# Performance work log

Hardware: AMD Instinct MI355X
Metric: run time of the kernel (lower is better)

The kernel has to match this reference:

```python
import jax, jax.numpy as jnp
import numpy as np

B, L, N, C, H = 32, 11, 577, 768, 12
HD = C // H  # head dim 64
THRESH = 0.5
NEG = -1e9


def layer_norm(x, g, b, eps=1e-6):
    m = jnp.mean(x, axis=-1, keepdims=True)
    v = jnp.var(x, axis=-1, keepdims=True)
    return (x - m) * jax.lax.rsqrt(v + eps) * g + b


def setup_inputs() -> dict:
    key = jax.random.key(0)
    ks = jax.random.split(key, 8)
    s = 0.02
    return {
        "last_x": jax.random.normal(ks[0], (B, N, C), jnp.float32),
        "attn_scores": jax.random.normal(ks[1], (B, L, N), jnp.float32),
        "norm1_g": jnp.ones((C,), jnp.float32),
        "norm1_b": jnp.zeros((C,), jnp.float32),
        "qkv_w": jax.random.normal(ks[2], (3 * C, C), jnp.float32) * s,
        "qkv_b": jnp.zeros((3 * C,), jnp.float32),
        "proj_w": jax.random.normal(ks[3], (C, C), jnp.float32) * s,
        "proj_b": jnp.zeros((C,), jnp.float32),
        "norm2_g": jnp.ones((C,), jnp.float32),
        "norm2_b": jnp.zeros((C,), jnp.float32),
        "fc1_w": jax.random.normal(ks[4], (4 * C, C), jnp.float32) * s,
        "fc1_b": jnp.zeros((4 * C,), jnp.float32),
        "fc2_w": jax.random.normal(ks[5], (C, 4 * C), jnp.float32) * s,
        "fc2_b": jnp.zeros((C,), jnp.float32),
        "bbn_g": jnp.ones((C,), jnp.float32),
        "bbn_b": jnp.zeros((C,), jnp.float32),
        "out_g": jnp.ones((C,), jnp.float32),
        "out_b": jnp.zeros((C,), jnp.float32),
    }


def prune(attn_scores):
    # scores per block, drop CLS column, softmax over patches, mean over blocks
    ps = jax.nn.softmax(attn_scores[:, :, 1:], axis=-1).mean(axis=1)  # [B, P]
    order = jnp.argsort(ps, axis=1)  # ascending
    sorted_s = jnp.take_along_axis(ps, order, axis=1)
    keep_sorted = jnp.cumsum(sorted_s, axis=1) > THRESH  # drop low-mass prefix
    # scatter back to original patch positions
    pm = jnp.zeros_like(keep_sorted)
    pm = pm.at[jnp.arange(ps.shape[0])[:, None], order].set(keep_sorted)
    # CLS token always kept
    return jnp.concatenate([jnp.ones((ps.shape[0], 1), bool), pm], axis=1)  # [B, N]


def masked_block(x, token_masks, norm1_g, norm1_b, qkv_w, qkv_b, proj_w, proj_b,
                 norm2_g, norm2_b, fc1_w, fc1_b, fc2_w, fc2_b):
    b, n, c = x.shape
    h = layer_norm(x, norm1_g, norm1_b)
    qkv = (h @ qkv_w.T + qkv_b).reshape(b, n, 3, H, HD).transpose(2, 0, 3, 1, 4)
    q, k, v = qkv[0], qkv[1], qkv[2]  # [B, H, N, HD]
    att = jnp.einsum("bhqd,bhkd->bhqk", q, k) * (HD ** -0.5)
    mf = token_masks.astype(x.dtype)
    pair = (mf[:, None, :, None] * mf[:, None, None, :]) > 0  # [B,1,N,N]
    att = jnp.where(pair, att, NEG)
    p = jax.nn.softmax(att, axis=-1)
    p = jnp.where(pair, p, 0.0)  # zero fully-masked rows
    y = jnp.einsum("bhqk,bhkd->bhqd", p, v).transpose(0, 2, 1, 3).reshape(b, n, c)
    y = y @ proj_w.T + proj_b
    x = x + y
    m = layer_norm(x, norm2_g, norm2_b)
    m = jax.nn.gelu(m @ fc1_w.T + fc1_b, approximate=False) @ fc2_w.T + fc2_b
    return x + m


def reference(last_x, attn_scores, norm1_g, norm1_b, qkv_w, qkv_b, proj_w, proj_b,
              norm2_g, norm2_b, fc1_w, fc1_b, fc2_w, fc2_b, bbn_g, bbn_b, out_g, out_b):
    token_masks = prune(attn_scores)  # [B, N] bool
    x = masked_block(last_x, token_masks, norm1_g, norm1_b, qkv_w, qkv_b,
                     proj_w, proj_b, norm2_g, norm2_b, fc1_w, fc1_b, fc2_w, fc2_b)
    x = layer_norm(x, bbn_g, bbn_b)  # backbone final norm
    mf = token_masks.astype(x.dtype)
    pooled = (x * mf[:, :, None]).sum(axis=1) / mf.sum(axis=1, keepdims=True)
    return layer_norm(pooled, out_g, out_b)  # [B, C]
```

## Files before the change

### kernel.cpp

```cpp
#include <hip/hip_runtime.h>

#define B_   32
#define L_   11
#define N_   577
#define C_   768
#define H_   12
#define HD_  64
#define M_   (B_ * N_)
#define NP_  608
#define QT_  16
#define NQT_ 37
#define MCH_ 4616

typedef unsigned int uint32;

typedef short bf16x8 __attribute__((ext_vector_type(8)));
typedef float f32x4  __attribute__((ext_vector_type(4)));

__device__ __forceinline__ unsigned short f2bf(float f) {
    union { float f; uint32 u; } c; c.f = f;
    uint32 u = c.u;
    uint32 r = (u + 0x7FFFu + ((u >> 16) & 1u)) >> 16;
    return (unsigned short)r;
}
__device__ __forceinline__ float bf2f(unsigned short u) {
    union { uint32 u; float f; } c; c.u = ((uint32)u) << 16;
    return c.f;
}
__device__ __forceinline__ float ldval(const float* p, size_t i) { return p[i]; }
__device__ __forceinline__ float ldval(const unsigned short* p, size_t i) { return bf2f(p[i]); }

__device__ __forceinline__ bf16x8 ld_frag(const unsigned short* p) {
    union { uint4 u; bf16x8 v; } c;
    c.u = *reinterpret_cast<const uint4*>(p);
    return c.v;
}

__device__ __forceinline__ void gload_lds16(const unsigned short* g, unsigned short* l) {
    __builtin_amdgcn_global_load_lds(
        (const __attribute__((address_space(1))) unsigned int*)g,
        (__attribute__((address_space(3))) unsigned int*)l, 16, 0, 0);
}

__global__ __launch_bounds__(256) void cast4_kernel(const float* __restrict__ qkvw,
                                                    const float* __restrict__ projw,
                                                    const float* __restrict__ fc1w,
                                                    const float* __restrict__ fc2w,
                                                    unsigned short* __restrict__ dq,
                                                    unsigned short* __restrict__ dp,
                                                    unsigned short* __restrict__ d1,
                                                    unsigned short* __restrict__ d2) {
    int i = blockIdx.x * 256 + threadIdx.x;
    const int N0 = 442368, N1 = 147456, N2 = 589824;
    const float* s; unsigned short* d; int j;
    if (i < N0)                { s = qkvw; d = dq; j = i; }
    else if (i < N0 + N1)      { s = projw; d = dp; j = i - N0; }
    else if (i < N0 + N1 + N2) { s = fc1w;  d = d1; j = i - N0 - N1; }
    else                       { s = fc2w;  d = d2; j = i - N0 - N1 - N2; }
    float4 v = reinterpret_cast<const float4*>(s)[j];
    union { unsigned short us[4]; uint2 u; } o;
    o.us[0] = f2bf(v.x); o.us[1] = f2bf(v.y); o.us[2] = f2bf(v.z); o.us[3] = f2bf(v.w);
    reinterpret_cast<uint2*>(d)[j] = o.u;
}

__global__ __launch_bounds__(256) void prune_kernel(const float* __restrict__ scores,
                                                    float* __restrict__ maskf,
                                                    float* __restrict__ cnt) {
    int b = blockIdx.x, tid = threadIdx.x;
    int lane = tid & 63, wave = tid >> 6;
    __shared__ float ps[576];
    __shared__ float red[4];
    for (int j = tid; j < 576; j += 256) ps[j] = 0.f;
    __syncthreads();
    for (int l = 0; l < L_; ++l) {
        const float* row = scores + ((size_t)b * L_ + l) * N_ + 1;
        float mx = -3.4e38f;
        for (int j = tid; j < 576; j += 256) mx = fmaxf(mx, row[j]);
        for (int off = 32; off; off >>= 1) mx = fmaxf(mx, __shfl_xor(mx, off));
        if (lane == 0) red[wave] = mx;
        __syncthreads();
        mx = fmaxf(fmaxf(red[0], red[1]), fmaxf(red[2], red[3]));
        __syncthreads();
        float s = 0.f;
        for (int j = tid; j < 576; j += 256) s += expf(row[j] - mx);
        for (int off = 32; off; off >>= 1) s += __shfl_xor(s, off);
        if (lane == 0) red[wave] = s;
        __syncthreads();
        s = red[0] + red[1] + red[2] + red[3];
        float inv = 1.f / s;
        for (int j = tid; j < 576; j += 256) ps[j] += expf(row[j] - mx) * inv;
        __syncthreads();
    }
    for (int j = tid; j < 576; j += 256) ps[j] = ps[j] / 11.0f;
    __syncthreads();
    int kept = 0;
    for (int i = tid; i < 576; i += 256) {
        float vi = ps[i];
        float s = 0.f;
        for (int j = 0; j < 576; ++j) {
            float vj = ps[j];
            if (vj < vi || (vj == vi && j <= i)) s += vj;
        }
        int k = (s > 0.5f) ? 1 : 0;
        maskf[b * N_ + 1 + i] = (float)k;
        kept += k;
    }
    __syncthreads();
    for (int off = 32; off; off >>= 1) kept += __shfl_xor(kept, off);
    if (lane == 0) red[wave] = (float)kept;
    __syncthreads();
    if (tid == 0) {
        cnt[b] = red[0] + red[1] + red[2] + red[3] + 1.f;
        maskf[b * N_] = 1.f;
    }
}

template<typename T>
__global__ __launch_bounds__(256) void ln_kernel(const T* __restrict__ x,
                                                 const float* __restrict__ g,
                                                 const float* __restrict__ bta,
                                                 unsigned short* __restrict__ dst_bf,
                                                 float* __restrict__ mu_out,
                                                 float* __restrict__ rs_out) {
    int row = blockIdx.x, tid = threadIdx.x;
    int lane = tid & 63, wave = tid >> 6;
    const T* xr = x + (size_t)row * C_;
    __shared__ float s1[4], s2[4];
    float s = 0.f, sq = 0.f;
    for (int c = tid; c < C_; c += 256) { float v = ldval(xr, c); s += v; sq += v * v; }
    for (int off = 32; off; off >>= 1) { s += __shfl_xor(s, off); sq += __shfl_xor(sq, off); }
    if (lane == 0) { s1[wave] = s; s2[wave] = sq; }
    __syncthreads();
    float ts = s1[0] + s1[1] + s1[2] + s1[3];
    float tq = s2[0] + s2[1] + s2[2] + s2[3];
    float mean = ts / (float)C_;
    float var = tq / (float)C_ - mean * mean;
    float rs = rsqrtf(var + 1e-6f);
    if (mu_out && tid == 0) { mu_out[row] = mean; rs_out[row] = rs; }
    if (dst_bf) {
        for (int c = tid; c < C_; c += 256) {
            float v = (ldval(xr, c) - mean) * rs * g[c] + bta[c];
            dst_bf[(size_t)row * C_ + c] = f2bf(v);
        }
    }
}

template<int MODE, int MI>
__global__ __launch_bounds__(256) void gemm_kernel(const unsigned short* __restrict__ A,
                                                   const unsigned short* __restrict__ Bm,
                                                   const float* __restrict__ bias,
                                                   const float* __restrict__ residf,
                                                   const unsigned short* __restrict__ residb,
                                                   unsigned short* __restrict__ outb,
                                                   unsigned short* __restrict__ qd,
                                                   unsigned short* __restrict__ kd,
                                                   unsigned short* __restrict__ vd,
                                                   int M, int N, int K) {
    constexpr int TILE = MI * 32;
    __shared__ unsigned short As[TILE * 32];
    __shared__ unsigned short Bs[TILE * 32];
    int bid = blockIdx.x;
    int NT = N / TILE;
    int mt = bid / NT, nt = bid % NT;
    int m0 = mt * TILE, n0 = nt * TILE;
    int tid = threadIdx.x, lane = tid & 63, wave = tid >> 6;
    int ml = lane & 15, quad = lane >> 4;
    int srow = wave * 16 + (lane >> 2);
    int skc = (lane & 3) * 8;
    const unsigned short* ag[MI / 2 == 0 ? 1 : MI / 2];
    const unsigned short* bg[MI / 2 == 0 ? 1 : MI / 2];
#pragma unroll
    for (int jj = 0; jj < MI / 2; ++jj) {
        ag[jj] = A + (size_t)min(m0 + jj * 64 + srow, M - 1) * K + skc;
        bg[jj] = Bm + (size_t)(n0 + jj * 64 + srow) * K + skc;
    }
    int msub = (wave & 1) * (MI * 16), nsub = (wave >> 1) * (MI * 16);
    f32x4 acc[MI][MI] = {};
    for (int k0 = 0; k0 < K; k0 += 32) {
        __syncthreads();
#pragma unroll
        for (int jj = 0; jj < MI / 2; ++jj) {
            gload_lds16(ag[jj] + k0, As + jj * 2048 + wave * 512);
            gload_lds16(bg[jj] + k0, Bs + jj * 2048 + wave * 512);
        }
        asm volatile("s_waitcnt vmcnt(0)" ::: "memory");
        __syncthreads();
        bf16x8 af[MI], bfm[MI];
#pragma unroll
        for (int i = 0; i < MI; ++i) af[i] = ld_frag(As + (msub + 16 * i + ml) * 32 + quad * 8);
#pragma unroll
        for (int j = 0; j < MI; ++j) bfm[j] = ld_frag(Bs + (nsub + 16 * j + ml) * 32 + quad * 8);
#pragma unroll
        for (int i = 0; i < MI; ++i)
#pragma unroll
            for (int j = 0; j < MI; ++j)
                acc[i][j] = __builtin_amdgcn_mfma_f32_16x16x32_bf16(af[i], bfm[j], acc[i][j], 0, 0, 0);
    }
#pragma unroll
    for (int i = 0; i < MI; ++i)
#pragma unroll
    for (int j = 0; j < MI; ++j)
#pragma unroll
    for (int r = 0; r < 4; ++r) {
        int row = m0 + msub + 16 * i + quad * 4 + r;
        if (row >= M) continue;
        int col = n0 + nsub + 16 * j + ml;
        float v = acc[i][j][r] + bias[col];
        if (MODE == 0) {
            int b = row / N_, t = row - b * N_;
            int f = col;
            if (f < 768) {
                qd[((size_t)(b * H_ + (f >> 6)) * N_ + t) * HD_ + (f & 63)] = f2bf(v * 0.125f);
            } else if (f < 1536) {
                f -= 768;
                kd[((size_t)(b * H_ + (f >> 6)) * N_ + t) * HD_ + (f & 63)] = f2bf(v);
            } else {
                f -= 1536;
                vd[((size_t)(b * H_ + (f >> 6)) * HD_ + (f & 63)) * NP_ + t] = f2bf(v);
            }
        } else if (MODE == 1) {
            outb[(size_t)row * N + col] = f2bf(v + residf[(size_t)row * N + col]);
        } else if (MODE == 2) {
            float gl = 0.5f * v * (1.f + erff(v * 0.70710678118654752f));
            outb[(size_t)row * N + col] = f2bf(gl);
        } else {
            outb[(size_t)row * N + col] = f2bf(v + bf2f(residb[(size_t)row * N + col]));
        }
    }
}

__global__ __launch_bounds__(256, 4) void attn_kernel(const unsigned short* __restrict__ qb,
                                                      const unsigned short* __restrict__ kb,
                                                      const unsigned short* __restrict__ vt,
                                                      const float* __restrict__ maskf,
                                                      unsigned short* __restrict__ ybf) {
    int bid = blockIdx.x;
    int xcd = bid & 7, g = bid >> 3;
    int bh = (g / NQT_) * 8 + xcd;
    int qt = g % NQT_;
    int h = bh % H_, b = bh / H_;
    int q0 = qt * QT_;
    int tid = threadIdx.x, lane = tid & 63, wave = tid >> 6;
    int ml = lane & 15, quad = lane >> 4, kq = quad * 8;
    __shared__ __align__(16) unsigned short P[QT_][616];
    __shared__ float wred[4][QT_];

    const float* bmask = maskf + (size_t)b * N_;
    float mrowv[4];
#pragma unroll
    for (int r = 0; r < 4; ++r) {
        int t = q0 + quad * 4 + r;
        mrowv[r] = (t < N_) ? bmask[t] : 0.f;
    }
    const unsigned short* qbase = qb + (size_t)(b * H_ + h) * N_ * HD_;
    const unsigned short* kbase = kb + (size_t)(b * H_ + h) * N_ * HD_;
    int qrow = min(q0 + ml, N_ - 1);
    bf16x8 aq0 = ld_frag(qbase + (size_t)qrow * HD_ + kq);
    bf16x8 aq1 = ld_frag(qbase + (size_t)qrow * HD_ + kq + 32);
    float sreg[10][4];
    float ls[4] = {0.f, 0.f, 0.f, 0.f};
#pragma unroll
    for (int t = 0; t < 10; ++t) {
        int nt = wave + 4 * t;
        if (nt < NP_ / 16) {
            int col = nt * 16 + ml;
            int krow = min(col, N_ - 1);
            bf16x8 bk0 = ld_frag(kbase + (size_t)krow * HD_ + kq);
            bf16x8 bk1 = ld_frag(kbase + (size_t)krow * HD_ + kq + 32);
            f32x4 a = {0.f, 0.f, 0.f, 0.f};
            a = __builtin_amdgcn_mfma_f32_16x16x32_bf16(aq0, bk0, a, 0, 0, 0);
            a = __builtin_amdgcn_mfma_f32_16x16x32_bf16(aq1, bk1, a, 0, 0, 0);
            bool keep = (col < N_) && (bmask[col] > 0.f);
#pragma unroll
            for (int r = 0; r < 4; ++r) {
                float e = keep ? __expf(a[r]) : 0.f;
                sreg[t][r] = e;
                ls[r] += e;
            }
        } else {
#pragma unroll
            for (int r = 0; r < 4; ++r) sreg[t][r] = 0.f;
        }
    }
#pragma unroll
    for (int r = 0; r < 4; ++r) {
#pragma unroll
        for (int off = 1; off < 16; off <<= 1) ls[r] += __shfl_xor(ls[r], off);
    }
    if (ml == 0) {
#pragma unroll
        for (int r = 0; r < 4; ++r) wred[wave][quad * 4 + r] = ls[r];
    }
#pragma unroll
    for (int t = 0; t < 10; ++t) {
        int nt = wave + 4 * t;
        if (nt < NP_ / 16) {
#pragma unroll
            for (int r = 0; r < 4; ++r) P[quad * 4 + r][nt * 16 + ml] = f2bf(sreg[t][r]);
        }
    }
    __syncthreads();
    float inv[4];
#pragma unroll
    for (int r = 0; r < 4; ++r) {
        int row = quad * 4 + r;
        float sum = wred[0][row] + wred[1][row] + wred[2][row] + wred[3][row];
        inv[r] = mrowv[r] / sum;
    }
    const unsigned short* vrow = vt + ((size_t)(b * H_ + h) * HD_ + wave * 16 + ml) * NP_ + kq;
    f32x4 acc = {0.f, 0.f, 0.f, 0.f};
#pragma unroll
    for (int t = 0; t < 19; ++t) {
        bf16x8 pa = ld_frag(&P[ml][kq + t * 32]);
        bf16x8 vb = ld_frag(vrow + t * 32);
        acc = __builtin_amdgcn_mfma_f32_16x16x32_bf16(pa, vb, acc, 0, 0, 0);
    }
#pragma unroll
    for (int r = 0; r < 4; ++r) {
        int t = q0 + quad * 4 + r;
        if (t < N_)
            ybf[((size_t)(b * N_ + t)) * C_ + h * HD_ + wave * 16 + ml] = f2bf(acc[r] * inv[r]);
    }
}

__global__ __launch_bounds__(256) void pool_kernel(const unsigned short* __restrict__ x2,
                                                   const float* __restrict__ mu,
                                                   const float* __restrict__ rs,
                                                   const float* __restrict__ maskf,
                                                   float* __restrict__ praw) {
    int c = blockIdx.x * 256 + threadIdx.x;
    int tchunk = blockIdx.y;
    int b = blockIdx.z;
    int t0 = tchunk * 73, t1 = min(t0 + 73, N_);
    float s = 0.f;
    for (int t = t0; t < t1; ++t) {
        int row = b * N_ + t;
        float m = maskf[row];
        if (m > 0.f) s += (bf2f(x2[(size_t)row * C_ + c]) - mu[row]) * rs[row];
    }
    atomicAdd(&praw[b * C_ + c], s);
}

__global__ __launch_bounds__(256) void final_kernel(const float* __restrict__ praw,
                                                    const float* __restrict__ cnt,
                                                    const float* __restrict__ bg,
                                                    const float* __restrict__ bb,
                                                    const float* __restrict__ og,
                                                    const float* __restrict__ ob,
                                                    float* __restrict__ out) {
    int b = blockIdx.x, tid = threadIdx.x;
    int lane = tid & 63, wave = tid >> 6;
    __shared__ float u[C_];
    __shared__ float r1[4], r2[4];
    float inv = 1.f / cnt[b];
    float s = 0.f, sq = 0.f;
    for (int c = tid; c < C_; c += 256) {
        float v = bg[c] * praw[b * C_ + c] * inv + bb[c];
        u[c] = v; s += v; sq += v * v;
    }
    for (int off = 32; off; off >>= 1) { s += __shfl_xor(s, off); sq += __shfl_xor(sq, off); }
    if (lane == 0) { r1[wave] = s; r2[wave] = sq; }
    __syncthreads();
    float ts = r1[0] + r1[1] + r1[2] + r1[3];
    float tq = r2[0] + r2[1] + r2[2] + r2[3];
    float mean = ts / (float)C_;
    float var = tq / (float)C_ - mean * mean;
    float rstd = rsqrtf(var + 1e-6f);
    for (int c = tid; c < C_; c += 256)
        out[b * C_ + c] = (u[c] - mean) * rstd * og[c] + ob[c];
}

extern "C" void kernel_launch(void* const* d_in, const int* in_sizes, int n_in,
                              void* d_out, int out_size, void* d_ws, size_t ws_size,
                              hipStream_t stream) {
    const float* last_x  = (const float*)d_in[0];
    const float* scores  = (const float*)d_in[1];
    const float* n1g     = (const float*)d_in[2];
    const float* n1b     = (const float*)d_in[3];
    const float* qkv_w   = (const float*)d_in[4];
    const float* qkv_b   = (const float*)d_in[5];
    const float* proj_w  = (const float*)d_in[6];
    const float* proj_b  = (const float*)d_in[7];
    const float* n2g     = (const float*)d_in[8];
    const float* n2b     = (const float*)d_in[9];
    const float* fc1_w   = (const float*)d_in[10];
    const float* fc1_b   = (const float*)d_in[11];
    const float* fc2_w   = (const float*)d_in[12];
    const float* fc2_b   = (const float*)d_in[13];
    const float* bbn_g   = (const float*)d_in[14];
    const float* bbn_b   = (const float*)d_in[15];
    const float* out_g   = (const float*)d_in[16];
    const float* out_b   = (const float*)d_in[17];
    float* out = (float*)d_out;

    char* w = (char*)d_ws;
    size_t off = 0;
    auto alloc = [&](size_t bytes) -> char* {
        off = (off + 255) & ~(size_t)255;
        char* p = w + off;
        off += bytes;
        return p;
    };
    unsigned short* wq = (unsigned short*)alloc((size_t)2304 * 768 * 2);
    unsigned short* wp = (unsigned short*)alloc((size_t)768 * 768 * 2);
    unsigned short* w1 = (unsigned short*)alloc((size_t)3072 * 768 * 2);
    unsigned short* w2 = (unsigned short*)alloc((size_t)768 * 3072 * 2);
    float* maskf = (float*)alloc((size_t)M_ * 4);
    float* cnt   = (float*)alloc(32 * 4);
    float* mu    = (float*)alloc((size_t)M_ * 4);
    float* rs    = (float*)alloc((size_t)M_ * 4);
    float* praw  = (float*)alloc((size_t)B_ * C_ * 4);
    unsigned short* h_bf = (unsigned short*)alloc((size_t)M_ * C_ * 2);
    unsigned short* q_bf = (unsigned short*)alloc((size_t)B_ * H_ * N_ * HD_ * 2);
    unsigned short* k_bf = (unsigned short*)alloc((size_t)B_ * H_ * N_ * HD_ * 2);
    unsigned short* vt   = (unsigned short*)alloc((size_t)B_ * H_ * HD_ * NP_ * 2);
    unsigned short* y_bf = h_bf;
    unsigned short* m_bf = q_bf;
    unsigned short* x1   = vt;
    unsigned short* x2   = k_bf;

    size_t act_need = (size_t)M_ * 3072 * 2;
    bool big = (((off + 255) & ~(size_t)255) + act_need) <= ws_size;
    unsigned short* act = big ? (unsigned short*)alloc(act_need) : h_bf;

    cast4_kernel<<<6912, 256, 0, stream>>>(qkv_w, proj_w, fc1_w, fc2_w, wq, wp, w1, w2);
    prune_kernel<<<B_, 256, 0, stream>>>(scores, maskf, cnt);
    ln_kernel<float><<<M_, 256, 0, stream>>>(last_x, n1g, n1b, h_bf, nullptr, nullptr);
    gemm_kernel<0, 4><<<((M_ + 127) / 128) * (2304 / 128), 256, 0, stream>>>(
        h_bf, wq, qkv_b, nullptr, nullptr, nullptr, q_bf, k_bf, vt, M_, 2304, C_);
    attn_kernel<<<B_ * H_ * NQT_, 256, 0, stream>>>(q_bf, k_bf, vt, maskf, y_bf);
    gemm_kernel<1, 4><<<((M_ + 127) / 128) * (768 / 128), 256, 0, stream>>>(
        y_bf, wp, proj_b, last_x, nullptr, x1, nullptr, nullptr, nullptr, M_, C_, C_);
    ln_kernel<unsigned short><<<M_, 256, 0, stream>>>(x1, n2g, n2b, m_bf, nullptr, nullptr);
    if (big) {
        gemm_kernel<2, 4><<<((M_ + 127) / 128) * (3072 / 128), 256, 0, stream>>>(
            m_bf, w1, fc1_b, nullptr, nullptr, act, nullptr, nullptr, nullptr, M_, 3072, C_);
        gemm_kernel<3, 4><<<((M_ + 127) / 128) * (768 / 128), 256, 0, stream>>>(
            act, w2, fc2_b, nullptr, x1, x2, nullptr, nullptr, nullptr, M_, C_, 3072);
    } else {
        for (int c = 0; c < 4; ++c) {
            int r0 = c * MCH_;
            gemm_kernel<2, 4><<<((MCH_ + 127) / 128) * (3072 / 128), 256, 0, stream>>>(
                m_bf + (size_t)r0 * C_, w1, fc1_b, nullptr, nullptr, act,
                nullptr, nullptr, nullptr, MCH_, 3072, C_);
            gemm_kernel<3, 4><<<((MCH_ + 127) / 128) * (768 / 128), 256, 0, stream>>>(
                act, w2, fc2_b, nullptr, x1 + (size_t)r0 * C_, x2 + (size_t)r0 * C_,
                nullptr, nullptr, nullptr, MCH_, 768, 3072);
        }
    }
    ln_kernel<unsigned short><<<M_, 256, 0, stream>>>(x2, bbn_g, bbn_b, nullptr, mu, rs);
    hipMemsetAsync(praw, 0, (size_t)B_ * C_ * 4, stream);
    dim3 pg(3, 8, B_);
    pool_kernel<<<pg, 256, 0, stream>>>(x2, mu, rs, maskf, praw);
    final_kernel<<<B_, 256, 0, stream>>>(praw, cnt, bbn_g, bbn_b, out_g, out_b, out);
    (void)in_sizes; (void)n_in; (void)out_size;
}
```

Measured before the change: 1.215 ms.

## Double query tile in attention and stage two K-chunks per GEMM sync

The attention kernel now processes 32 query rows per block in two 16-row subtiles, reusing each loaded K fragment and V fragment for both and writing P straight to shared memory instead of holding scores in registers. The GEMM kernel loads two 32-wide K chunks into separate LDS buffers per iteration, halving barriers and waits per unit of K. These cut global K/V traffic and synchronisation overhead. The cost is larger LDS and register use per block and fewer attention blocks, which may reduce occupancy.

```diff
diff --git a/kernel.cpp b/kernel.cpp
--- a/kernel.cpp
+++ b/kernel.cpp
@@ -8,8 +8,8 @@
 #define HD_  64
 #define M_   (B_ * N_)
 #define NP_  608
-#define QT_  16
-#define NQT_ 37
+#define QT_  32
+#define NQT_ 19
 #define MCH_ 4616
 
 typedef unsigned int uint32;
@@ -157,8 +157,8 @@
                                                    unsigned short* __restrict__ vd,
                                                    int M, int N, int K) {
     constexpr int TILE = MI * 32;
-    __shared__ unsigned short As[TILE * 32];
-    __shared__ unsigned short Bs[TILE * 32];
+    __shared__ unsigned short As[2][TILE * 32];
+    __shared__ unsigned short Bs[2][TILE * 32];
     int bid = blockIdx.x;
     int NT = N / TILE;
     int mt = bid / NT, nt = bid % NT;
@@ -176,25 +176,30 @@
     }
     int msub = (wave & 1) * (MI * 16), nsub = (wave >> 1) * (MI * 16);
     f32x4 acc[MI][MI] = {};
-    for (int k0 = 0; k0 < K; k0 += 32) {
-        __syncthreads();
+    for (int k0 = 0; k0 < K; k0 += 64) {
+        __syncthreads();
+#pragma unroll
+        for (int c = 0; c < 2; ++c)
 #pragma unroll
         for (int jj = 0; jj < MI / 2; ++jj) {
-            gload_lds16(ag[jj] + k0, As + jj * 2048 + wave * 512);
-            gload_lds16(bg[jj] + k0, Bs + jj * 2048 + wave * 512);
+            gload_lds16(ag[jj] + k0 + c * 32, As[c] + jj * 2048 + wave * 512);
+            gload_lds16(bg[jj] + k0 + c * 32, Bs[c] + jj * 2048 + wave * 512);
         }
         asm volatile("s_waitcnt vmcnt(0)" ::: "memory");
         __syncthreads();
-        bf16x8 af[MI], bfm[MI];
-#pragma unroll
-        for (int i = 0; i < MI; ++i) af[i] = ld_frag(As + (msub + 16 * i + ml) * 32 + quad * 8);
-#pragma unroll
-        for (int j = 0; j < MI; ++j) bfm[j] = ld_frag(Bs + (nsub + 16 * j + ml) * 32 + quad * 8);
-#pragma unroll
-        for (int i = 0; i < MI; ++i)
-#pragma unroll
-            for (int j = 0; j < MI; ++j)
-                acc[i][j] = __builtin_amdgcn_mfma_f32_16x16x32_bf16(af[i], bfm[j], acc[i][j], 0, 0, 0);
+#pragma unroll
+        for (int c = 0; c < 2; ++c) {
+            bf16x8 af[MI], bfm[MI];
+#pragma unroll
+            for (int i = 0; i < MI; ++i) af[i] = ld_frag(As[c] + (msub + 16 * i + ml) * 32 + quad * 8);
+#pragma unroll
+            for (int j = 0; j < MI; ++j) bfm[j] = ld_frag(Bs[c] + (nsub + 16 * j + ml) * 32 + quad * 8);
+#pragma unroll
+            for (int i = 0; i < MI; ++i)
+#pragma unroll
+                for (int j = 0; j < MI; ++j)
+                    acc[i][j] = __builtin_amdgcn_mfma_f32_16x16x32_bf16(af[i], bfm[j], acc[i][j], 0, 0, 0);
+        }
     }
 #pragma unroll
     for (int i = 0; i < MI; ++i)
@@ -246,19 +251,24 @@
     __shared__ float wred[4][QT_];
 
     const float* bmask = maskf + (size_t)b * N_;
-    float mrowv[4];
+    float mrowv[2][4];
+#pragma unroll
+    for (int s = 0; s < 2; ++s)
 #pragma unroll
     for (int r = 0; r < 4; ++r) {
-        int t = q0 + quad * 4 + r;
-        mrowv[r] = (t < N_) ? bmask[t] : 0.f;
+        int t = q0 + s * 16 + quad * 4 + r;
+        mrowv[s][r] = (t < N_) ? bmask[t] : 0.f;
     }
     const unsigned short* qbase = qb + (size_t)(b * H_ + h) * N_ * HD_;
     const unsigned short* kbase = kb + (size_t)(b * H_ + h) * N_ * HD_;
-    int qrow = min(q0 + ml, N_ - 1);
-    bf16x8 aq0 = ld_frag(qbase + (size_t)qrow * HD_ + kq);
-    bf16x8 aq1 = ld_frag(qbase + (size_t)qrow * HD_ + kq + 32);
-    float sreg[10][4];
-    float ls[4] = {0.f, 0.f, 0.f, 0.f};
+    bf16x8 aq[2][2];
+#pragma unroll
+    for (int s = 0; s < 2; ++s) {
+        int qrow = min(q0 + s * 16 + ml, N_ - 1);
+        aq[s][0] = ld_frag(qbase + (size_t)qrow * HD_ + kq);
+        aq[s][1] = ld_frag(qbase + (size_t)qrow * HD_ + kq + 32);
+    }
+    float ls[2][4] = {};
 #pragma unroll
     for (int t = 0; t < 10; ++t) {
         int nt = wave + 4 * t;
@@ -267,59 +277,62 @@
             int krow = min(col, N_ - 1);
             bf16x8 bk0 = ld_frag(kbase + (size_t)krow * HD_ + kq);
             bf16x8 bk1 = ld_frag(kbase + (size_t)krow * HD_ + kq + 32);
-            f32x4 a = {0.f, 0.f, 0.f, 0.f};
-            a = __builtin_amdgcn_mfma_f32_16x16x32_bf16(aq0, bk0, a, 0, 0, 0);
-            a = __builtin_amdgcn_mfma_f32_16x16x32_bf16(aq1, bk1, a, 0, 0, 0);
             bool keep = (col < N_) && (bmask[col] > 0.f);
 #pragma unroll
-            for (int r = 0; r < 4; ++r) {
-                float e = keep ? __expf(a[r]) : 0.f;
-                sreg[t][r] = e;
-                ls[r] += e;
+            for (int s = 0; s < 2; ++s) {
+                f32x4 a = {0.f, 0.f, 0.f, 0.f};
+                a = __builtin_amdgcn_mfma_f32_16x16x32_bf16(aq[s][0], bk0, a, 0, 0, 0);
+                a = __builtin_amdgcn_mfma_f32_16x16x32_bf16(aq[s][1], bk1, a, 0, 0, 0);
+#pragma unroll
+                for (int r = 0; r < 4; ++r) {
+                    float e = keep ? __expf(a[r]) : 0.f;
+                    ls[s][r] += e;
+                    P[s * 16 + quad * 4 + r][col] = f2bf(e);
+                }
             }
-        } else {
-#pragma unroll
-            for (int r = 0; r < 4; ++r) sreg[t][r] = 0.f;
-        }
-    }
+        }
+    }
+#pragma unroll
+    for (int s = 0; s < 2; ++s)
 #pragma unroll
     for (int r = 0; r < 4; ++r) {
 #pragma unroll
-        for (int off = 1; off < 16; off <<= 1) ls[r] += __shfl_xor(ls[r], off);
+        for (int off = 1; off < 16; off <<= 1) ls[s][r] += __shfl_xor(ls[s][r], off);
     }
     if (ml == 0) {
 #pragma unroll
-        for (int r = 0; r < 4; ++r) wred[wave][quad * 4 + r] = ls[r];
-    }
-#pragma unroll
-    for (int t = 0; t < 10; ++t) {
-        int nt = wave + 4 * t;
-        if (nt < NP_ / 16) {
-#pragma unroll
-            for (int r = 0; r < 4; ++r) P[quad * 4 + r][nt * 16 + ml] = f2bf(sreg[t][r]);
-        }
-    }
-    __syncthreads();
-    float inv[4];
+        for (int s = 0; s < 2; ++s)
+#pragma unroll
+        for (int r = 0; r < 4; ++r) wred[wave][s * 16 + quad * 4 + r] = ls[s][r];
+    }
+    __syncthreads();
+    float inv[2][4];
+#pragma unroll
+    for (int s = 0; s < 2; ++s)
 #pragma unroll
     for (int r = 0; r < 4; ++r) {
-        int row = quad * 4 + r;
+        int row = s * 16 + quad * 4 + r;
         float sum = wred[0][row] + wred[1][row] + wred[2][row] + wred[3][row];
-        inv[r] = mrowv[r] / sum;
+        inv[s][r] = mrowv[s][r] / sum;
     }
     const unsigned short* vrow = vt + ((size_t)(b * H_ + h) * HD_ + wave * 16 + ml) * NP_ + kq;
-    f32x4 acc = {0.f, 0.f, 0.f, 0.f};
+    f32x4 acc[2] = {};
 #pragma unroll
     for (int t = 0; t < 19; ++t) {
-        bf16x8 pa = ld_frag(&P[ml][kq + t * 32]);
         bf16x8 vb = ld_frag(vrow + t * 32);
-        acc = __builtin_amdgcn_mfma_f32_16x16x32_bf16(pa, vb, acc, 0, 0, 0);
-    }
+#pragma unroll
+        for (int s = 0; s < 2; ++s) {
+            bf16x8 pa = ld_frag(&P[s * 16 + ml][kq + t * 32]);
+            acc[s] = __builtin_amdgcn_mfma_f32_16x16x32_bf16(pa, vb, acc[s], 0, 0, 0);
+        }
+    }
+#pragma unroll
+    for (int s = 0; s < 2; ++s)
 #pragma unroll
     for (int r = 0; r < 4; ++r) {
-        int t = q0 + quad * 4 + r;
+        int t = q0 + s * 16 + quad * 4 + r;
         if (t < N_)
-            ybf[((size_t)(b * N_ + t)) * C_ + h * HD_ + wave * 16 + ml] = f2bf(acc[r] * inv[r]);
+            ybf[((size_t)(b * N_ + t)) * C_ + h * HD_ + wave * 16 + ml] = f2bf(acc[s][r] * inv[s][r]);
     }
 }
 
```

New measurement: 1.169 ms. 3.8% less time.
